# Kernel optimization log

Hardware: AMD Instinct MI355X
Metric: run time of the kernel (lower is better)

Reference implementation:

```python
import jax, jax.numpy as jnp
import numpy as np


def setup_inputs() -> dict:
    key = jax.random.key(0)
    ks = jax.random.split(key, 11)
    B, Cin, H, W = 4, 3, 256, 256
    width, m1, m2, L = 64, 16, 16, 4
    def n(k, shape, scale=1.0):
        return (scale * jax.random.normal(k, shape)).astype(jnp.float32)
    spec_scale = 1.0 / (width * width)  # matches torch scale = 1/(in_ch*out_ch)
    return {
        "x": n(ks[0], (B, Cin, H, W)),
        "fc0_w": n(ks[1], (width, Cin), 0.1),
        "fc0_b": n(ks[2], (width,), 0.1),
        "spec_wr": n(ks[3], (L, width, width, m1, m2), spec_scale),
        "spec_wi": n(ks[4], (L, width, width, m1, m2), spec_scale),
        "w_w": n(ks[5], (L, width, width), 0.1),
        "w_b": n(ks[6], (L, width), 0.1),
        "fc1_w": n(ks[7], (128, width), 0.1),
        "fc1_b": n(ks[8], (128,), 0.1),
        "fc2_w": n(ks[9], (1, 128), 0.1),
        "fc2_b": n(ks[10], (1,), 0.1),
    }


def conv1x1(x, w, b):
    # x: (B,C,H,W), w: (O,C), b: (O,) -- equivalent to nn.Conv2d(C,O,1)
    return jnp.einsum('bchw,oc->bohw', x, w) + b[None, :, None, None]


def spectral_conv2d(x, wr, wi):
    # x: (B,C,H,W); wr/wi: (C,O,m1,m2) real/imag parts of cfloat weight
    B, C, H, W = x.shape
    m1, m2 = wr.shape[2], wr.shape[3]
    O = wr.shape[1]
    x_ft = jnp.fft.rfft2(x)                       # (B,C,H,W//2+1) complex64
    w = wr + 1j * wi
    blk = jnp.einsum('bixy,ioxy->boxy', x_ft[:, :, :m1, :m2], w)
    out_ft = jnp.zeros((B, O, H, W // 2 + 1), dtype=blk.dtype)
    out_ft = out_ft.at[:, :, :m1, :m2].set(blk)
    return jnp.fft.irfft2(out_ft, s=(H, W))


def reference(x, fc0_w, fc0_b, spec_wr, spec_wi, w_w, w_b, fc1_w, fc1_b, fc2_w, fc2_b):
    h = conv1x1(x, fc0_w, fc0_b)
    n_layers = spec_wr.shape[0]
    for i in range(n_layers):
        h = spectral_conv2d(h, spec_wr[i], spec_wi[i]) + conv1x1(h, w_w[i], w_b[i])
        h = jax.nn.gelu(h, approximate=False)
    h = jax.nn.gelu(conv1x1(h, fc1_w, fc1_b), approximate=False)
    return conv1x1(h, fc2_w, fc2_b)
```

## Files before the change

kernel.cpp:

```cpp
#include <hip/hip_runtime.h>
#include <math.h>

#define HW 65536

typedef __attribute__((ext_vector_type(8))) short short8;
typedef __attribute__((ext_vector_type(4))) float f32x4;

__device__ __forceinline__ unsigned bf16rne(float f) {
  union { float f; unsigned u; } a; a.f = f;
  return (a.u + 0x7fffu + ((a.u >> 16) & 1u)) >> 16;
}
__device__ __forceinline__ float bf16tof(unsigned h) {
  union { unsigned u; float f; } a; a.u = h << 16;
  return a.f;
}
__device__ __forceinline__ float gelu(float v) {
  float ax = fabsf(v) * 0.70710678118654752f;
  float t = 1.0f / fmaf(0.3275911f, ax, 1.0f);
  float p = t * (0.254829592f +
           t * (-0.284496736f +
           t * (1.421413741f +
           t * (-1.453152027f +
           t * 1.061405429f))));
  float e = __expf(-ax * ax);
  float er = copysignf(fmaf(-p, e, 1.0f), v);
  return 0.5f * v * (1.0f + er);
}

__global__ __launch_bounds__(256) void k_tables(float* __restrict__ cosT, float* __restrict__ sinT,
                                                ushort* __restrict__ eah, ushort* __restrict__ eal,
                                                ushort* __restrict__ e2h, ushort* __restrict__ e2l,
                                                const float* __restrict__ ww, const float* __restrict__ w1,
                                                ushort* __restrict__ wh, ushort* __restrict__ wl,
                                                ushort* __restrict__ w1h, ushort* __restrict__ w1l) {
  int idx = blockIdx.x * 256 + threadIdx.x;
  const float w = 0.0245436926061702596f;
  if (idx < 4096) {
    int k = idx >> 8, xx = idx & 255;
    int t = (k * xx) & 255;
    float ang = (float)t * w;
    cosT[idx] = cosf(ang);
    sinT[idx] = sinf(ang);
  } else if (idx < 12288) {
    int e = idx - 4096;
    int j = e >> 8, xx = e & 255;
    int k = j >> 1;
    int t = (k * xx) & 255;
    float ang = (float)t * w;
    float val = (j & 1) ? -sinf(ang) : cosf(ang);
    unsigned hi = bf16rne(val);
    unsigned lo = bf16rne(val - bf16tof(hi));
    eah[j * 256 + xx] = (ushort)hi;
    eal[j * 256 + xx] = (ushort)lo;
    e2h[xx * 32 + j] = (ushort)hi;
    e2l[xx * 32 + j] = (ushort)lo;
  } else if (idx < 28672) {
    int j = idx - 12288;
    float v = ww[j];
    unsigned hi = bf16rne(v);
    wh[j] = (ushort)hi;
    wl[j] = (ushort)bf16rne(v - bf16tof(hi));
  } else {
    int j = idx - 28672;
    float v = w1[j];
    unsigned hi = bf16rne(v);
    w1h[j] = (ushort)hi;
    w1l[j] = (ushort)bf16rne(v - bf16tof(hi));
  }
}

__global__ __launch_bounds__(256) void k_fc0(const float* __restrict__ x, const float* __restrict__ w,
                                             const float* __restrict__ b,
                                             const ushort* __restrict__ eah, const ushort* __restrict__ eal,
                                             ushort* __restrict__ hh, float* __restrict__ A2) {
  int bid = blockIdx.x;
  int bb = bid >> 8, y = bid & 255;
  int tid = threadIdx.x;
  __shared__ float ws[192];
  __shared__ float bs[64];
  __shared__ __align__(16) ushort XsH[256 * 66];
  if (tid < 192) ws[tid] = w[tid];
  if (tid < 64) bs[tid] = b[tid];
  __syncthreads();
  const float* xrow = x + ((size_t)(bb * 3) * 256 + y) * 256;
#pragma unroll
  for (int rep = 0; rep < 8; ++rep) {
    int flat = rep * 256 + tid;
    int p = flat >> 3, q = flat & 7;
    float v0 = xrow[p], v1 = xrow[p + HW], v2 = xrow[p + 2 * HW];
    short8 H;
#pragma unroll
    for (int i = 0; i < 8; ++i) {
      int o = q * 8 + i;
      float v = bs[o] + ws[o * 3] * v0 + ws[o * 3 + 1] * v1 + ws[o * 3 + 2] * v2;
      H[i] = (short)bf16rne(v);
    }
    size_t nb = ((size_t)bid * 256 + p) * 64 + q * 8;
    *(short8*)&hh[nb] = H;
    *(short8*)&XsH[p * 66 + q * 8] = H;
  }
  __syncthreads();
  int lane = tid & 63, wv = tid >> 6;
  int lm = lane & 15, lg = lane >> 4;
#pragma unroll
  for (int ntile = 0; ntile < 4; ++ntile) {
    f32x4 dacc[2];
    dacc[0] = (f32x4){0.f, 0.f, 0.f, 0.f};
    dacc[1] = (f32x4){0.f, 0.f, 0.f, 0.f};
#pragma unroll
    for (int kstep = 0; kstep < 2; ++kstep) {
      int x0 = wv * 64 + kstep * 32 + lg * 8;
      short8 bh;
#pragma unroll
      for (int i = 0; i < 8; ++i) {
        bh[i] = (short)XsH[(x0 + i) * 66 + ntile * 16 + lm];
      }
#pragma unroll
      for (int mtile = 0; mtile < 2; ++mtile) {
        short8 ah = *(const short8*)&eah[(mtile * 16 + lm) * 256 + x0];
        short8 al = *(const short8*)&eal[(mtile * 16 + lm) * 256 + x0];
        dacc[mtile] = __builtin_amdgcn_mfma_f32_16x16x32_bf16(ah, bh, dacc[mtile], 0, 0, 0);
        dacc[mtile] = __builtin_amdgcn_mfma_f32_16x16x32_bf16(al, bh, dacc[mtile], 0, 0, 0);
      }
    }
    int c = ntile * 16 + lm;
    size_t row = ((size_t)(bb * 64 + c) * 256 + y) * 128 + wv * 32 + lg * 8;
    *(float4*)&A2[row] = make_float4(dacc[0][0], dacc[0][1], dacc[0][2], dacc[0][3]);
    *(float4*)&A2[row + 4] = make_float4(dacc[1][0], dacc[1][1], dacc[1][2], dacc[1][3]);
  }
}

__global__ __launch_bounds__(256) void k_f2(const float* __restrict__ A2, const float* __restrict__ cosT,
                                            const float* __restrict__ sinT, float2* __restrict__ X) {
  int plane = blockIdx.x;
  int tid = threadIdx.x;
  __shared__ float2 As[256 * 16];
  __shared__ float ct[16 * 257];
  __shared__ float stt[16 * 257];
  const float* Ap = A2 + (size_t)plane * 256 * 128;
#pragma unroll
  for (int rep = 0; rep < 16; ++rep) {
    int flat = rep * 256 + tid;
    int y = flat >> 4, j = flat & 15;
    int twoj = 2 * j;
    int s = ((twoj >> 2) & 3) * 8 + (twoj >> 4) * 4 + (twoj & 3);
    float2 v = make_float2(0.f, 0.f);
#pragma unroll
    for (int q = 0; q < 4; ++q) {
      float2 a = *(const float2*)&Ap[y * 128 + q * 32 + s];
      v.x += a.x; v.y += a.y;
    }
    As[y * 16 + j] = v;
  }
#pragma unroll
  for (int rep = 0; rep < 16; ++rep) {
    int flat = rep * 256 + tid;
    int ky = flat >> 8, y = flat & 255;
    ct[ky * 257 + y] = cosT[flat];
    stt[ky * 257 + y] = sinT[flat];
  }
  __syncthreads();
  int ky = tid >> 4, kx = tid & 15;
  float xr = 0.f, xi = 0.f;
#pragma unroll 4
  for (int y = 0; y < 256; ++y) {
    float2 a = As[y * 16 + kx];
    float c = ct[ky * 257 + y], s = stt[ky * 257 + y];
    xr += c * a.x + s * a.y;
    xi += c * a.y - s * a.x;
  }
  X[plane * 256 + tid] = make_float2(xr, xi);
}

__global__ __launch_bounds__(256) void k_mix(const float2* __restrict__ X, const float* __restrict__ wr,
                                             const float* __restrict__ wi, float2* __restrict__ Y) {
  int o = blockIdx.x >> 2;
  int mc = blockIdx.x & 3;
  int tid = threadIdx.x;
  int cg = tid >> 6, m2 = tid & 63;
  int m = mc * 64 + m2;
  float yr[4] = {0.f, 0.f, 0.f, 0.f}, yi[4] = {0.f, 0.f, 0.f, 0.f};
#pragma unroll 4
  for (int cc = 0; cc < 16; ++cc) {
    int c = cg * 16 + cc;
    float r = wr[(c * 64 + o) * 256 + m];
    float im = wi[(c * 64 + o) * 256 + m];
#pragma unroll
    for (int b = 0; b < 4; ++b) {
      float2 xv = X[(b * 64 + c) * 256 + m];
      yr[b] += xv.x * r - xv.y * im;
      yi[b] += xv.x * im + xv.y * r;
    }
  }
  __shared__ float2 red[1024];
#pragma unroll
  for (int b = 0; b < 4; ++b) red[cg * 256 + b * 64 + m2] = make_float2(yr[b], yi[b]);
  __syncthreads();
  int b = tid >> 6;
  float sx = 0.f, sy = 0.f;
#pragma unroll
  for (int g2 = 0; g2 < 4; ++g2) {
    float2 v = red[g2 * 256 + b * 64 + m2];
    sx += v.x; sy += v.y;
  }
  Y[(b * 64 + o) * 256 + m] = make_float2(sx, sy);
}

__global__ __launch_bounds__(256) void k_inv1(const float2* __restrict__ Y, const float* __restrict__ cosT,
                                              const float* __restrict__ sinT,
                                              ushort* __restrict__ gh, ushort* __restrict__ gl) {
  int plane = blockIdx.x;
  int y = threadIdx.x;
  __shared__ float2 Ys[256];
  Ys[threadIdx.x] = Y[plane * 256 + threadIdx.x];
  __syncthreads();
  float gr[16], gi[16];
#pragma unroll
  for (int k = 0; k < 16; ++k) { gr[k] = 0.f; gi[k] = 0.f; }
  for (int ky = 0; ky < 16; ++ky) {
    float c = cosT[ky * 256 + y], s = sinT[ky * 256 + y];
#pragma unroll
    for (int kx = 0; kx < 16; ++kx) {
      float2 v = Ys[ky * 16 + kx];
      gr[kx] += c * v.x - s * v.y;
      gi[kx] += c * v.y + s * v.x;
    }
  }
  float val[32];
  const float sc = 1.0f / 65536.0f;
#pragma unroll
  for (int kx = 0; kx < 16; ++kx) {
    float m = (kx == 0) ? sc : 2.0f * sc;
    val[2 * kx] = gr[kx] * m;
    val[2 * kx + 1] = gi[kx] * m;
  }
  size_t gb = ((size_t)plane * 256 + y) * 32;
#pragma unroll
  for (int q = 0; q < 8; ++q) {
    ushort4 H, L;
#pragma unroll
    for (int r = 0; r < 4; ++r) {
      float v = val[q * 4 + r];
      unsigned hi = bf16rne(v);
      ((ushort*)&H)[r] = (ushort)hi;
      ((ushort*)&L)[r] = (ushort)bf16rne(v - bf16tof(hi));
    }
    *(ushort4*)&gh[gb + q * 4] = H;
    *(ushort4*)&gl[gb + q * 4] = L;
  }
}

__global__ __launch_bounds__(256) void k_layer(const ushort* __restrict__ hh,
                                               const ushort* __restrict__ gh, const ushort* __restrict__ gl,
                                               const ushort* __restrict__ wh, const ushort* __restrict__ wl,
                                               const float* __restrict__ wb,
                                               const ushort* __restrict__ e2h, const ushort* __restrict__ e2l,
                                               const ushort* __restrict__ eah, const ushort* __restrict__ eal,
                                               ushort* __restrict__ oh,
                                               float* __restrict__ A2, int do_dft) {
  int bid = blockIdx.x;
  int b = bid >> 10, y = (bid >> 2) & 255, xq = bid & 3;
  int tid = threadIdx.x;
  int lane = tid & 63, wave = tid >> 6;
  int lm = lane & 15, lg = lane >> 4;
  int x = xq * 64 + wave * 16 + lm;
  size_t nb = (size_t)(b * 256 + y) * 256 + x;

  __shared__ __align__(16) ushort wsH[64 * 72], wsL[64 * 72];
  __shared__ __align__(16) ushort gsH[64 * 40], gsL[64 * 40];
  __shared__ __align__(16) ushort esH[64 * 40], esL[64 * 40];
  __shared__ float wbs[64];

#pragma unroll
  for (int rep = 0; rep < 2; ++rep) {
    int flat = rep * 2048 + tid * 8;
    int o = flat >> 6, cc = flat & 63;
    *(short8*)&wsH[o * 72 + cc] = *(const short8*)&wh[flat];
    *(short8*)&wsL[o * 72 + cc] = *(const short8*)&wl[flat];
  }
  {
    int o = tid >> 2, i = (tid & 3) * 8;
    size_t ga = ((size_t)(b * 64 + o) * 256 + y) * 32 + i;
    *(short8*)&gsH[o * 40 + i] = *(const short8*)&gh[ga];
    *(short8*)&gsL[o * 40 + i] = *(const short8*)&gl[ga];
  }
  {
    int xr = tid >> 2, i = (tid & 3) * 8;
    int ea = (xq * 64 + xr) * 32 + i;
    *(short8*)&esH[xr * 40 + i] = *(const short8*)&e2h[ea];
    *(short8*)&esL[xr * 40 + i] = *(const short8*)&e2l[ea];
  }
  if (tid < 64) wbs[tid] = wb[tid];
  __syncthreads();

  short8 bh0 = *(const short8*)&hh[nb * 64 + lg * 8];
  short8 bh1 = *(const short8*)&hh[nb * 64 + 32 + lg * 8];
  int xr = wave * 16 + lm;
  short8 eh = *(const short8*)&esH[xr * 40 + lg * 8];
  short8 el = *(const short8*)&esL[xr * 40 + lg * 8];

  f32x4 acc[4];
#pragma unroll
  for (int mi = 0; mi < 4; ++mi) acc[mi] = (f32x4){0.f, 0.f, 0.f, 0.f};

#pragma unroll
  for (int mi = 0; mi < 4; ++mi) {
    int o = mi * 16 + lm;
    short8 ah0 = *(const short8*)&wsH[o * 72 + lg * 8];
    short8 al0 = *(const short8*)&wsL[o * 72 + lg * 8];
    acc[mi] = __builtin_amdgcn_mfma_f32_16x16x32_bf16(ah0, bh0, acc[mi], 0, 0, 0);
    acc[mi] = __builtin_amdgcn_mfma_f32_16x16x32_bf16(al0, bh0, acc[mi], 0, 0, 0);
    short8 ah1 = *(const short8*)&wsH[o * 72 + 32 + lg * 8];
    short8 al1 = *(const short8*)&wsL[o * 72 + 32 + lg * 8];
    acc[mi] = __builtin_amdgcn_mfma_f32_16x16x32_bf16(ah1, bh1, acc[mi], 0, 0, 0);
    acc[mi] = __builtin_amdgcn_mfma_f32_16x16x32_bf16(al1, bh1, acc[mi], 0, 0, 0);
    short8 gah = *(const short8*)&gsH[o * 40 + lg * 8];
    short8 gal = *(const short8*)&gsL[o * 40 + lg * 8];
    acc[mi] = __builtin_amdgcn_mfma_f32_16x16x32_bf16(gah, eh, acc[mi], 0, 0, 0);
    acc[mi] = __builtin_amdgcn_mfma_f32_16x16x32_bf16(gah, el, acc[mi], 0, 0, 0);
    acc[mi] = __builtin_amdgcn_mfma_f32_16x16x32_bf16(gal, eh, acc[mi], 0, 0, 0);
  }

  __syncthreads();
  int xl = wave * 16 + lm;
#pragma unroll
  for (int mi = 0; mi < 4; ++mi) {
    ushort4 H;
#pragma unroll
    for (int r = 0; r < 4; ++r) {
      int o = mi * 16 + lg * 4 + r;
      float ge = gelu(acc[mi][r] + wbs[o]);
      ((ushort*)&H)[r] = (ushort)bf16rne(ge);
    }
    *(ushort4*)&wsH[xl * 66 + mi * 16 + lg * 4] = H;
  }
  __syncthreads();
  size_t rowbase = (size_t)(b * 256 + y) * 256 + xq * 64;
#pragma unroll
  for (int rep = 0; rep < 2; ++rep) {
    int ch = rep * 256 + tid;
    int p = ch >> 3, off = (ch & 7) * 8;
    short8 vH = *(const short8*)&wsH[p * 66 + off];
    *(short8*)&oh[(rowbase + p) * 64 + off] = vH;
  }

  if (do_dft) {
    f32x4 dacc[2];
    dacc[0] = (f32x4){0.f, 0.f, 0.f, 0.f};
    dacc[1] = (f32x4){0.f, 0.f, 0.f, 0.f};
#pragma unroll
    for (int kstep = 0; kstep < 2; ++kstep) {
      int xls = kstep * 32 + lg * 8;
      short8 bh;
#pragma unroll
      for (int i = 0; i < 8; ++i) {
        bh[i] = (short)wsH[(xls + i) * 66 + wave * 16 + lm];
      }
      int x0g = xq * 64 + xls;
#pragma unroll
      for (int mtile = 0; mtile < 2; ++mtile) {
        short8 ah = *(const short8*)&eah[(mtile * 16 + lm) * 256 + x0g];
        short8 al = *(const short8*)&eal[(mtile * 16 + lm) * 256 + x0g];
        dacc[mtile] = __builtin_amdgcn_mfma_f32_16x16x32_bf16(ah, bh, dacc[mtile], 0, 0, 0);
        dacc[mtile] = __builtin_amdgcn_mfma_f32_16x16x32_bf16(al, bh, dacc[mtile], 0, 0, 0);
      }
    }
    int c = wave * 16 + lm;
    size_t row = ((size_t)(b * 64 + c) * 256 + y) * 128 + xq * 32 + lg * 8;
    *(float4*)&A2[row] = make_float4(dacc[0][0], dacc[0][1], dacc[0][2], dacc[0][3]);
    *(float4*)&A2[row + 4] = make_float4(dacc[1][0], dacc[1][1], dacc[1][2], dacc[1][3]);
  }
}

__global__ __launch_bounds__(256) void k_final(const ushort* __restrict__ hh,
                                               const ushort* __restrict__ w1h, const ushort* __restrict__ w1l,
                                               const float* __restrict__ b1, const float* __restrict__ w2,
                                               const float* __restrict__ b2, float* __restrict__ out) {
  int bid = blockIdx.x;
  int b = bid >> 10, y = (bid >> 2) & 255, xq = bid & 3;
  int tid = threadIdx.x;
  int lane = tid & 63, wave = tid >> 6;
  int lm = lane & 15, lg = lane >> 4;
  int x = xq * 64 + wave * 16 + lm;
  size_t nb = (size_t)(b * 256 + y) * 256 + x;

  __shared__ __align__(16) ushort w1sH[128 * 72], w1sL[128 * 72];
  __shared__ float b1s[128], w2s[128];

#pragma unroll
  for (int rep = 0; rep < 4; ++rep) {
    int flat = rep * 2048 + tid * 8;
    int j = flat >> 6, cc = flat & 63;
    *(short8*)&w1sH[j * 72 + cc] = *(const short8*)&w1h[flat];
    *(short8*)&w1sL[j * 72 + cc] = *(const short8*)&w1l[flat];
  }
  if (tid < 128) { b1s[tid] = b1[tid]; w2s[tid] = w2[tid]; }
  __syncthreads();

  short8 bh0 = *(const short8*)&hh[nb * 64 + lg * 8];
  short8 bh1 = *(const short8*)&hh[nb * 64 + 32 + lg * 8];

  f32x4 acc[8];
#pragma unroll
  for (int mi = 0; mi < 8; ++mi) acc[mi] = (f32x4){0.f, 0.f, 0.f, 0.f};

#pragma unroll
  for (int mi = 0; mi < 8; ++mi) {
    int j = mi * 16 + lm;
    short8 ah0 = *(const short8*)&w1sH[j * 72 + lg * 8];
    short8 al0 = *(const short8*)&w1sL[j * 72 + lg * 8];
    acc[mi] = __builtin_amdgcn_mfma_f32_16x16x32_bf16(ah0, bh0, acc[mi], 0, 0, 0);
    acc[mi] = __builtin_amdgcn_mfma_f32_16x16x32_bf16(al0, bh0, acc[mi], 0, 0, 0);
    short8 ah1 = *(const short8*)&w1sH[j * 72 + 32 + lg * 8];
    short8 al1 = *(const short8*)&w1sL[j * 72 + 32 + lg * 8];
    acc[mi] = __builtin_amdgcn_mfma_f32_16x16x32_bf16(ah1, bh1, acc[mi], 0, 0, 0);
    acc[mi] = __builtin_amdgcn_mfma_f32_16x16x32_bf16(al1, bh1, acc[mi], 0, 0, 0);
  }

  float p = 0.f;
#pragma unroll
  for (int mi = 0; mi < 8; ++mi)
#pragma unroll
    for (int r = 0; r < 4; ++r) {
      int j = mi * 16 + lg * 4 + r;
      p += w2s[j] * gelu(acc[mi][r] + b1s[j]);
    }
  p += __shfl_xor(p, 16);
  p += __shfl_xor(p, 32);
  if (lg == 0) {
    out[(b * 256 + y) * 256 + x] = p + b2[0];
  }
}

extern "C" void kernel_launch(void* const* d_in, const int* in_sizes, int n_in,
                              void* d_out, int out_size, void* d_ws, size_t ws_size,
                              hipStream_t stream) {
  const float* x       = (const float*)d_in[0];
  const float* fc0_w   = (const float*)d_in[1];
  const float* fc0_b   = (const float*)d_in[2];
  const float* spec_wr = (const float*)d_in[3];
  const float* spec_wi = (const float*)d_in[4];
  const float* w_w     = (const float*)d_in[5];
  const float* w_b     = (const float*)d_in[6];
  const float* fc1_w   = (const float*)d_in[7];
  const float* fc1_b   = (const float*)d_in[8];
  const float* fc2_w   = (const float*)d_in[9];
  const float* fc2_b   = (const float*)d_in[10];
  float* out = (float*)d_out;

  char* ws = (char*)d_ws;
  ushort* h0h  = (ushort*)ws;
  ushort* h1h  = (ushort*)(ws + 33554432);
  float*  A2   = (float*)(ws + 67108864);
  ushort* gh   = (ushort*)(ws + 100663296);
  ushort* gl   = (ushort*)(ws + 104857600);
  float2* X    = (float2*)(ws + 109051904);
  float2* Y    = (float2*)(ws + 109576192);
  float*  cosT = (float*)(ws + 110100480);
  float*  sinT = (float*)(ws + 110116864);
  ushort* eah  = (ushort*)(ws + 110133248);
  ushort* eal  = (ushort*)(ws + 110149632);
  ushort* e2h  = (ushort*)(ws + 110166016);
  ushort* e2l  = (ushort*)(ws + 110182400);
  ushort* wWh  = (ushort*)(ws + 110198784);
  ushort* wWl  = (ushort*)(ws + 110231552);
  ushort* w1h  = (ushort*)(ws + 110264320);
  ushort* w1l  = (ushort*)(ws + 110280704);

  k_tables<<<144, 256, 0, stream>>>(cosT, sinT, eah, eal, e2h, e2l,
                                    w_w, fc1_w, wWh, wWl, w1h, w1l);
  k_fc0<<<1024, 256, 0, stream>>>(x, fc0_w, fc0_b, eah, eal, h0h, A2);
  ushort* hch = h0h;
  ushort* hnh = h1h;
  for (int l = 0; l < 4; ++l) {
    k_f2<<<256, 256, 0, stream>>>(A2, cosT, sinT, X);
    k_mix<<<256, 256, 0, stream>>>(X, spec_wr + (size_t)l * 1048576, spec_wi + (size_t)l * 1048576, Y);
    k_inv1<<<256, 256, 0, stream>>>(Y, cosT, sinT, gh, gl);
    k_layer<<<4096, 256, 0, stream>>>(hch, gh, gl, wWh + l * 4096, wWl + l * 4096,
                                      w_b + l * 64, e2h, e2l, eah, eal, hnh, A2, (l < 3) ? 1 : 0);
    ushort* t = hch; hch = hnh; hnh = t;
  }
  k_final<<<4096, 256, 0, stream>>>(hch, w1h, w1l, fc1_b, fc2_w, fc2_b, out);
}
```

Before: 356.2 us.

## Split k_f2 over y halves and read spectral operands directly in k_layer

k_f2 now launches two blocks per plane, each reducing half of the y range into a partial result. k_mix sums the two partials when it loads X. This doubles the block count for the small DFT kernel, which with 256 blocks could not fill all CUs, and halves its shared memory per block. Separately, k_layer no longer stages the g and e2 tiles through LDS and loads them straight from global memory into registers, dropping shared-memory traffic and footprint at the cost of less coalesced global reads.

```diff
diff --git a/kernel.cpp b/kernel.cpp
--- a/kernel.cpp
+++ b/kernel.cpp
@@ -131,17 +131,19 @@
 }
 
 __global__ __launch_bounds__(256) void k_f2(const float* __restrict__ A2, const float* __restrict__ cosT,
-                                            const float* __restrict__ sinT, float2* __restrict__ X) {
-  int plane = blockIdx.x;
+                                            const float* __restrict__ sinT, float2* __restrict__ Xp) {
+  int bid = blockIdx.x;
+  int plane = bid >> 1, yh = bid & 1;
   int tid = threadIdx.x;
-  __shared__ float2 As[256 * 16];
-  __shared__ float ct[16 * 257];
-  __shared__ float stt[16 * 257];
+  __shared__ float2 As[128 * 16];
+  __shared__ float ct[16 * 129];
+  __shared__ float stt[16 * 129];
   const float* Ap = A2 + (size_t)plane * 256 * 128;
 #pragma unroll
-  for (int rep = 0; rep < 16; ++rep) {
+  for (int rep = 0; rep < 8; ++rep) {
     int flat = rep * 256 + tid;
-    int y = flat >> 4, j = flat & 15;
+    int yp = flat >> 4, j = flat & 15;
+    int y = yh * 128 + yp;
     int twoj = 2 * j;
     int s = ((twoj >> 2) & 3) * 8 + (twoj >> 4) * 4 + (twoj & 3);
     float2 v = make_float2(0.f, 0.f);
@@ -150,29 +152,29 @@
       float2 a = *(const float2*)&Ap[y * 128 + q * 32 + s];
       v.x += a.x; v.y += a.y;
     }
-    As[y * 16 + j] = v;
-  }
-#pragma unroll
-  for (int rep = 0; rep < 16; ++rep) {
+    As[yp * 16 + j] = v;
+  }
+#pragma unroll
+  for (int rep = 0; rep < 8; ++rep) {
     int flat = rep * 256 + tid;
-    int ky = flat >> 8, y = flat & 255;
-    ct[ky * 257 + y] = cosT[flat];
-    stt[ky * 257 + y] = sinT[flat];
+    int ky = flat >> 7, yp = flat & 127;
+    ct[ky * 129 + yp] = cosT[ky * 256 + yh * 128 + yp];
+    stt[ky * 129 + yp] = sinT[ky * 256 + yh * 128 + yp];
   }
   __syncthreads();
   int ky = tid >> 4, kx = tid & 15;
   float xr = 0.f, xi = 0.f;
 #pragma unroll 4
-  for (int y = 0; y < 256; ++y) {
-    float2 a = As[y * 16 + kx];
-    float c = ct[ky * 257 + y], s = stt[ky * 257 + y];
+  for (int yp = 0; yp < 128; ++yp) {
+    float2 a = As[yp * 16 + kx];
+    float c = ct[ky * 129 + yp], s = stt[ky * 129 + yp];
     xr += c * a.x + s * a.y;
     xi += c * a.y - s * a.x;
   }
-  X[plane * 256 + tid] = make_float2(xr, xi);
-}
-
-__global__ __launch_bounds__(256) void k_mix(const float2* __restrict__ X, const float* __restrict__ wr,
+  Xp[(size_t)plane * 512 + yh * 256 + tid] = make_float2(xr, xi);
+}
+
+__global__ __launch_bounds__(256) void k_mix(const float2* __restrict__ Xp, const float* __restrict__ wr,
                                              const float* __restrict__ wi, float2* __restrict__ Y) {
   int o = blockIdx.x >> 2;
   int mc = blockIdx.x & 3;
@@ -187,9 +189,12 @@
     float im = wi[(c * 64 + o) * 256 + m];
 #pragma unroll
     for (int b = 0; b < 4; ++b) {
-      float2 xv = X[(b * 64 + c) * 256 + m];
-      yr[b] += xv.x * r - xv.y * im;
-      yi[b] += xv.x * im + xv.y * r;
+      size_t pb = (size_t)(b * 64 + c) * 512;
+      float2 x0 = Xp[pb + m];
+      float2 x1 = Xp[pb + 256 + m];
+      float xvx = x0.x + x1.x, xvy = x0.y + x1.y;
+      yr[b] += xvx * r - xvy * im;
+      yi[b] += xvx * im + xvy * r;
     }
   }
   __shared__ float2 red[1024];
@@ -267,8 +272,6 @@
   size_t nb = (size_t)(b * 256 + y) * 256 + x;
 
   __shared__ __align__(16) ushort wsH[64 * 72], wsL[64 * 72];
-  __shared__ __align__(16) ushort gsH[64 * 40], gsL[64 * 40];
-  __shared__ __align__(16) ushort esH[64 * 40], esL[64 * 40];
   __shared__ float wbs[64];
 
 #pragma unroll
@@ -278,26 +281,13 @@
     *(short8*)&wsH[o * 72 + cc] = *(const short8*)&wh[flat];
     *(short8*)&wsL[o * 72 + cc] = *(const short8*)&wl[flat];
   }
-  {
-    int o = tid >> 2, i = (tid & 3) * 8;
-    size_t ga = ((size_t)(b * 64 + o) * 256 + y) * 32 + i;
-    *(short8*)&gsH[o * 40 + i] = *(const short8*)&gh[ga];
-    *(short8*)&gsL[o * 40 + i] = *(const short8*)&gl[ga];
-  }
-  {
-    int xr = tid >> 2, i = (tid & 3) * 8;
-    int ea = (xq * 64 + xr) * 32 + i;
-    *(short8*)&esH[xr * 40 + i] = *(const short8*)&e2h[ea];
-    *(short8*)&esL[xr * 40 + i] = *(const short8*)&e2l[ea];
-  }
   if (tid < 64) wbs[tid] = wb[tid];
   __syncthreads();
 
   short8 bh0 = *(const short8*)&hh[nb * 64 + lg * 8];
   short8 bh1 = *(const short8*)&hh[nb * 64 + 32 + lg * 8];
-  int xr = wave * 16 + lm;
-  short8 eh = *(const short8*)&esH[xr * 40 + lg * 8];
-  short8 el = *(const short8*)&esL[xr * 40 + lg * 8];
+  short8 eh = *(const short8*)&e2h[x * 32 + lg * 8];
+  short8 el = *(const short8*)&e2l[x * 32 + lg * 8];
 
   f32x4 acc[4];
 #pragma unroll
@@ -314,8 +304,9 @@
     short8 al1 = *(const short8*)&wsL[o * 72 + 32 + lg * 8];
     acc[mi] = __builtin_amdgcn_mfma_f32_16x16x32_bf16(ah1, bh1, acc[mi], 0, 0, 0);
     acc[mi] = __builtin_amdgcn_mfma_f32_16x16x32_bf16(al1, bh1, acc[mi], 0, 0, 0);
-    short8 gah = *(const short8*)&gsH[o * 40 + lg * 8];
-    short8 gal = *(const short8*)&gsL[o * 40 + lg * 8];
+    size_t ga = ((size_t)(b * 64 + o) * 256 + y) * 32 + lg * 8;
+    short8 gah = *(const short8*)&gh[ga];
+    short8 gal = *(const short8*)&gl[ga];
     acc[mi] = __builtin_amdgcn_mfma_f32_16x16x32_bf16(gah, eh, acc[mi], 0, 0, 0);
     acc[mi] = __builtin_amdgcn_mfma_f32_16x16x32_bf16(gah, el, acc[mi], 0, 0, 0);
     acc[mi] = __builtin_amdgcn_mfma_f32_16x16x32_bf16(gal, eh, acc[mi], 0, 0, 0);
@@ -454,18 +445,18 @@
   float*  A2   = (float*)(ws + 67108864);
   ushort* gh   = (ushort*)(ws + 100663296);
   ushort* gl   = (ushort*)(ws + 104857600);
-  float2* X    = (float2*)(ws + 109051904);
-  float2* Y    = (float2*)(ws + 109576192);
-  float*  cosT = (float*)(ws + 110100480);
-  float*  sinT = (float*)(ws + 110116864);
-  ushort* eah  = (ushort*)(ws + 110133248);
-  ushort* eal  = (ushort*)(ws + 110149632);
-  ushort* e2h  = (ushort*)(ws + 110166016);
-  ushort* e2l  = (ushort*)(ws + 110182400);
-  ushort* wWh  = (ushort*)(ws + 110198784);
-  ushort* wWl  = (ushort*)(ws + 110231552);
-  ushort* w1h  = (ushort*)(ws + 110264320);
-  ushort* w1l  = (ushort*)(ws + 110280704);
+  float2* Xp   = (float2*)(ws + 109051904);
+  float2* Y    = (float2*)(ws + 110100480);
+  float*  cosT = (float*)(ws + 110624768);
+  float*  sinT = (float*)(ws + 110641152);
+  ushort* eah  = (ushort*)(ws + 110657536);
+  ushort* eal  = (ushort*)(ws + 110673920);
+  ushort* e2h  = (ushort*)(ws + 110690304);
+  ushort* e2l  = (ushort*)(ws + 110706688);
+  ushort* wWh  = (ushort*)(ws + 110723072);
+  ushort* wWl  = (ushort*)(ws + 110755840);
+  ushort* w1h  = (ushort*)(ws + 110788608);
+  ushort* w1l  = (ushort*)(ws + 110804992);
 
   k_tables<<<144, 256, 0, stream>>>(cosT, sinT, eah, eal, e2h, e2l,
                                     w_w, fc1_w, wWh, wWl, w1h, w1l);
@@ -473,8 +464,8 @@
   ushort* hch = h0h;
   ushort* hnh = h1h;
   for (int l = 0; l < 4; ++l) {
-    k_f2<<<256, 256, 0, stream>>>(A2, cosT, sinT, X);
-    k_mix<<<256, 256, 0, stream>>>(X, spec_wr + (size_t)l * 1048576, spec_wi + (size_t)l * 1048576, Y);
+    k_f2<<<512, 256, 0, stream>>>(A2, cosT, sinT, Xp);
+    k_mix<<<256, 256, 0, stream>>>(Xp, spec_wr + (size_t)l * 1048576, spec_wi + (size_t)l * 1048576, Y);
     k_inv1<<<256, 256, 0, stream>>>(Y, cosT, sinT, gh, gl);
     k_layer<<<4096, 256, 0, stream>>>(hch, gh, gl, wWh + l * 4096, wWl + l * 4096,
                                       w_b + l * 64, e2h, e2l, eah, eal, hnh, A2, (l < 3) ? 1 : 0);
```

Measured after the change: 367.5 us. +3.2%, slower.
